# Optimization experiments

Hardware: AMD Instinct MI355X
Metric: run time of the kernel (lower is better)

## Reference

```python
import jax, jax.numpy as jnp
import numpy as np

B, D = 4096, 512
STEPS = 50
LR, B1, B2, EPS = 0.01, 0.9, 0.999, 1e-8  # torch.optim.Adam defaults with lr=0.01


def setup_inputs() -> dict:
    key = jax.random.key(0)
    k1, k2, k3, k4 = jax.random.split(key, 4)
    s = jax.random.normal(k1, (B, D), dtype=jnp.float32)
    target_confidence = jax.random.uniform(k2, (B, 1), dtype=jnp.float32)
    # nn.Linear(style_dim, 1) init: U(-1/sqrt(D), 1/sqrt(D))
    lim = 1.0 / np.sqrt(D)
    W = jax.random.uniform(k3, (1, D), dtype=jnp.float32, minval=-lim, maxval=lim)
    b = jax.random.uniform(k4, (1,), dtype=jnp.float32, minval=-lim, maxval=lim)
    return {"s": s, "target_confidence": target_confidence, "W": W, "b": b}


def reference(s, target_confidence, W, b):
    # loss(x) = mse(sigmoid(x W^T + b), t) + l1(x, s); grad taken w.r.t. x only.
    def loss_fn(x):
        p = jax.nn.sigmoid(x @ W.T + b)                      # [B, 1]
        mse = jnp.mean((p - target_confidence) ** 2)
        d = x - s
        # stop_gradient(sign) so d|d|/dx = sign(d), with sign(0) = 0 (matches torch l1_loss subgradient)
        l1 = jnp.mean(jax.lax.stop_gradient(jnp.sign(d)) * d)
        return mse + l1

    grad_fn = jax.grad(loss_fn)

    def adam_step(carry, _):
        x, m, v, t = carry
        g = grad_fn(x)
        t = t + 1.0
        m = B1 * m + (1.0 - B1) * g
        v = B2 * v + (1.0 - B2) * g * g
        m_hat = m / (1.0 - B1 ** t)
        v_hat = v / (1.0 - B2 ** t)
        x = x - LR * m_hat / (jnp.sqrt(v_hat) + EPS)
        return (x, m, v, t), None

    init = (s, jnp.zeros_like(s), jnp.zeros_like(s), jnp.float32(0.0))
    (adjusted_s, _, _, _), _ = jax.lax.scan(adam_step, init, None, length=STEPS)
    return adjusted_s
```

## Files before the change

### kernel.cpp

```cpp
#include <hip/hip_runtime.h>

#define B_ 4096
#define D_ 512
#define STEPS_ 50

__device__ __forceinline__ float wave_reduce_add(float z) {
#pragma unroll
    for (int off = 32; off > 0; off >>= 1)
        z += __shfl_xor(z, off, 64);
    return z;
}

__global__ __launch_bounds__(256, 4) void adam_rows_kernel(
    const float* __restrict__ s,
    const float* __restrict__ tgt,
    const float* __restrict__ W,
    const float* __restrict__ bias_p,
    float* __restrict__ out)
{
    const int lane = threadIdx.x & 63;
    const int row  = (blockIdx.x << 2) + (threadIdx.x >> 6);

    const float4* srow4 = (const float4*)(s + (size_t)row * D_);
    const float4* W4    = (const float4*)W;

    float4 sa = srow4[lane];
    float4 sb = srow4[lane + 64];
    float4 wa = W4[lane];
    float4 wb = W4[lane + 64];
    const float b = bias_p[0];
    const float t = tgt[row];

    float ss[8] = {sa.x, sa.y, sa.z, sa.w, sb.x, sb.y, sb.z, sb.w};
    float ws[8] = {wa.x, wa.y, wa.z, wa.w, wb.x, wb.y, wb.z, wb.w};
    float dl[8], M[8], V[8];

    const float c_mse = 2.0f / (float)B_;
    const float c_l1  = 1.0f / ((float)B_ * (float)D_);
    const unsigned c_l1_bits = __float_as_uint(c_l1);

    float zs = 0.0f;
#pragma unroll
    for (int k = 0; k < 8; ++k) zs = fmaf(ss[k], ws[k], zs);
    zs = wave_reduce_add(zs);

    float pow1 = 0.9f, pow2 = 0.999f;

    {
        const float z    = zs + b;
        const float p    = __builtin_amdgcn_rcpf(1.0f + __expf(-z));
        const float coef = c_mse * (p - t) * p * (1.0f - p);
        const float A  = 0.001f * __builtin_amdgcn_rcpf(1.0f - pow1);
        const float u2 = 0.001f * __builtin_amdgcn_rcpf(1.0f - pow2);
#pragma unroll
        for (int k = 0; k < 8; ++k) {
            const float g = coef * ws[k];
            M[k] = g;
            V[k] = g * g;
            const float den = __builtin_amdgcn_sqrtf(V[k] * u2) + 1e-8f;
            dl[k] = -(A * M[k]) * __builtin_amdgcn_rcpf(den);
        }
    }

#pragma unroll 1
    for (int step = 1; step < STEPS_; ++step) {
        float dotd = 0.0f;
#pragma unroll
        for (int k = 0; k < 8; ++k) dotd = fmaf(dl[k], ws[k], dotd);
        dotd = wave_reduce_add(dotd);

        const float z    = (zs + dotd) + b;
        const float p    = __builtin_amdgcn_rcpf(1.0f + __expf(-z));
        const float coef = c_mse * (p - t) * p * (1.0f - p);

        pow1 *= 0.9f;
        pow2 *= 0.999f;
        const float A  = 0.001f * __builtin_amdgcn_rcpf(1.0f - pow1);
        const float u2 = 0.001f * __builtin_amdgcn_rcpf(1.0f - pow2);

#pragma unroll
        for (int k = 0; k < 8; ++k) {
            const unsigned sbit = __float_as_uint(dl[k]) & 0x80000000u;
            const float gl1 = __uint_as_float(sbit | c_l1_bits);
            const float g = fmaf(coef, ws[k], gl1);
            M[k] = fmaf(0.9f,   M[k], g);
            V[k] = fmaf(0.999f, V[k], g * g);
            const float den = __builtin_amdgcn_sqrtf(V[k] * u2) + 1e-8f;
            dl[k] = fmaf(-(A * M[k]), __builtin_amdgcn_rcpf(den), dl[k]);
        }
    }

    float4 oa = {ss[0] + dl[0], ss[1] + dl[1], ss[2] + dl[2], ss[3] + dl[3]};
    float4 ob = {ss[4] + dl[4], ss[5] + dl[5], ss[6] + dl[6], ss[7] + dl[7]};
    float4* orow4 = (float4*)(out + (size_t)row * D_);
    orow4[lane]      = oa;
    orow4[lane + 64] = ob;
}

extern "C" void kernel_launch(void* const* d_in, const int* in_sizes, int n_in,
                              void* d_out, int out_size, void* d_ws, size_t ws_size,
                              hipStream_t stream) {
    const float* s    = (const float*)d_in[0];
    const float* tgt  = (const float*)d_in[1];
    const float* W    = (const float*)d_in[2];
    const float* bias = (const float*)d_in[3];
    float* out = (float*)d_out;

    dim3 grid(B_ / 4), block(256);
    adam_rows_kernel<<<grid, block, 0, stream>>>(s, tgt, W, bias, out);
}
```

Measured before the change: 107.8 us.

## Use DPP wave reductions, one-wave blocks, and host-precomputed Adam bias-correction tables

Replaces the shfl_xor butterfly reduction with a DPP row_shr/row_bcast reduction followed by readlane, which moves the sum into a scalar register and avoids LDS-backed shuffles. Launches one 64-thread block per row instead of four rows per 256-thread block. Precomputes the per-step bias-correction factors on the host in double precision and passes them as a kernel-argument table, which removes per-step rcp calls in the serial loop. The tables are scalar constants, not activations, so this is legitimate. The smaller blocks may change scheduling or occupancy behaviour.

```diff
diff --git a/kernel.cpp b/kernel.cpp
--- a/kernel.cpp
+++ b/kernel.cpp
@@ -4,22 +4,32 @@
 #define D_ 512
 #define STEPS_ 50
 
-__device__ __forceinline__ float wave_reduce_add(float z) {
-#pragma unroll
-    for (int off = 32; off > 0; off >>= 1)
-        z += __shfl_xor(z, off, 64);
-    return z;
+struct BcTab { float negA[STEPS_]; float u2[STEPS_]; };
+
+#define DPP_ADD(x, ctrl) \
+    ((x) + __int_as_float(__builtin_amdgcn_update_dpp( \
+        0, __float_as_int(x), (ctrl), 0xf, 0xf, true)))
+
+__device__ __forceinline__ float wave64_sum(float x) {
+    x = DPP_ADD(x, 0x111);
+    x = DPP_ADD(x, 0x112);
+    x = DPP_ADD(x, 0x114);
+    x = DPP_ADD(x, 0x118);
+    x = DPP_ADD(x, 0x142);
+    x = DPP_ADD(x, 0x143);
+    return __int_as_float(__builtin_amdgcn_readlane(__float_as_int(x), 63));
 }
 
-__global__ __launch_bounds__(256, 4) void adam_rows_kernel(
+__global__ __launch_bounds__(64, 1) void adam_rows_kernel(
     const float* __restrict__ s,
     const float* __restrict__ tgt,
     const float* __restrict__ W,
     const float* __restrict__ bias_p,
-    float* __restrict__ out)
+    float* __restrict__ out,
+    const BcTab bc)
 {
-    const int lane = threadIdx.x & 63;
-    const int row  = (blockIdx.x << 2) + (threadIdx.x >> 6);
+    const int lane = threadIdx.x;
+    const int row  = blockIdx.x;
 
     const float4* srow4 = (const float4*)(s + (size_t)row * D_);
     const float4* W4    = (const float4*)W;
@@ -28,7 +38,6 @@
     float4 sb = srow4[lane + 64];
     float4 wa = W4[lane];
     float4 wb = W4[lane + 64];
-    const float b = bias_p[0];
     const float t = tgt[row];
 
     float ss[8] = {sa.x, sa.y, sa.z, sa.w, sb.x, sb.y, sb.z, sb.w};
@@ -36,29 +45,25 @@
     float dl[8], M[8], V[8];
 
     const float c_mse = 2.0f / (float)B_;
-    const float c_l1  = 1.0f / ((float)B_ * (float)D_);
-    const unsigned c_l1_bits = __float_as_uint(c_l1);
+    const unsigned c_l1_bits = 0x35000000u;
 
-    float zs = 0.0f;
+    float zdot = 0.0f;
 #pragma unroll
-    for (int k = 0; k < 8; ++k) zs = fmaf(ss[k], ws[k], zs);
-    zs = wave_reduce_add(zs);
-
-    float pow1 = 0.9f, pow2 = 0.999f;
+    for (int k = 0; k < 8; ++k) zdot = fmaf(ss[k], ws[k], zdot);
+    const float zb = wave64_sum(zdot) + bias_p[0];
 
     {
-        const float z    = zs + b;
-        const float p    = __builtin_amdgcn_rcpf(1.0f + __expf(-z));
+        const float p    = __builtin_amdgcn_rcpf(1.0f + __expf(-zb));
         const float coef = c_mse * (p - t) * p * (1.0f - p);
-        const float A  = 0.001f * __builtin_amdgcn_rcpf(1.0f - pow1);
-        const float u2 = 0.001f * __builtin_amdgcn_rcpf(1.0f - pow2);
+        const float negA = bc.negA[0];
+        const float u2   = bc.u2[0];
 #pragma unroll
         for (int k = 0; k < 8; ++k) {
             const float g = coef * ws[k];
             M[k] = g;
             V[k] = g * g;
             const float den = __builtin_amdgcn_sqrtf(V[k] * u2) + 1e-8f;
-            dl[k] = -(A * M[k]) * __builtin_amdgcn_rcpf(den);
+            dl[k] = (negA * M[k]) * __builtin_amdgcn_rcpf(den);
         }
     }
 
@@ -67,16 +72,12 @@
         float dotd = 0.0f;
 #pragma unroll
         for (int k = 0; k < 8; ++k) dotd = fmaf(dl[k], ws[k], dotd);
-        dotd = wave_reduce_add(dotd);
+        const float z = zb + wave64_sum(dotd);
 
-        const float z    = (zs + dotd) + b;
         const float p    = __builtin_amdgcn_rcpf(1.0f + __expf(-z));
         const float coef = c_mse * (p - t) * p * (1.0f - p);
-
-        pow1 *= 0.9f;
-        pow2 *= 0.999f;
-        const float A  = 0.001f * __builtin_amdgcn_rcpf(1.0f - pow1);
-        const float u2 = 0.001f * __builtin_amdgcn_rcpf(1.0f - pow2);
+        const float negA = bc.negA[step];
+        const float u2   = bc.u2[step];
 
 #pragma unroll
         for (int k = 0; k < 8; ++k) {
@@ -86,7 +87,7 @@
             M[k] = fmaf(0.9f,   M[k], g);
             V[k] = fmaf(0.999f, V[k], g * g);
             const float den = __builtin_amdgcn_sqrtf(V[k] * u2) + 1e-8f;
-            dl[k] = fmaf(-(A * M[k]), __builtin_amdgcn_rcpf(den), dl[k]);
+            dl[k] = fmaf(negA * M[k], __builtin_amdgcn_rcpf(den), dl[k]);
         }
     }
 
@@ -106,6 +107,13 @@
     const float* bias = (const float*)d_in[3];
     float* out = (float*)d_out;
 
-    dim3 grid(B_ / 4), block(256);
-    adam_rows_kernel<<<grid, block, 0, stream>>>(s, tgt, W, bias, out);
+    BcTab bc;
+    double p1 = 1.0, p2 = 1.0;
+    for (int t = 0; t < STEPS_; ++t) {
+        p1 *= 0.9; p2 *= 0.999;
+        bc.negA[t] = (float)(-0.001 / (1.0 - p1));
+        bc.u2[t]   = (float)( 0.001 / (1.0 - p2));
+    }
+
+    adam_rows_kernel<<<dim3(B_), dim3(64), 0, stream>>>(s, tgt, W, bias, out, bc);
 }
```

Result: faster. 100.3 us (-6.9%).
